# Kernel tuning notes

Hardware: AMD Instinct MI355X
Metric: run time of the kernel (lower is better)

Reference implementation:

```python
import jax, jax.numpy as jnp
import numpy as np

MEM_DIM, H, W = 1024, 16, 16
HW = H * W
N_TOKENS, BATCH = 8192, 8
C1, C2, EPS = 0.01, 0.03, 1e-8


def setup_inputs() -> dict:
    key = jax.random.key(0)
    ks = jax.random.split(key, 5)
    std_w = 1.0 / np.sqrt(HW)
    return {
        "input_tokens": jax.random.normal(ks[0], (N_TOKENS, BATCH, HW), dtype=jnp.float32),
        "memory": jax.random.normal(ks[1], (MEM_DIM, H, W), dtype=jnp.float32) * 0.1,
        "Wq": jax.random.normal(ks[2], (HW, HW), dtype=jnp.float32) * std_w,
        "Wk": jax.random.normal(ks[3], (HW, HW), dtype=jnp.float32) * std_w,
        "Wv": jax.random.normal(ks[4], (HW, HW), dtype=jnp.float32) * std_w,
    }


def _ssim(q, k):
    # q: [N, HW], k: [M, HW] -> ssim: [N, M]
    qm = jnp.mean(q, axis=1, keepdims=True)          # [N,1]
    km = jnp.mean(k, axis=1, keepdims=True)          # [M,1]
    qv = jnp.var(q, axis=1, ddof=1, keepdims=True)   # torch.var unbiased
    kv = jnp.var(k, axis=1, ddof=1, keepdims=True)
    cov = ((q - qm) @ (k - km).T) / (HW - 1)         # [N,M]
    mean_prod = qm @ km.T                            # [N,M]
    numerator = (2.0 * mean_prod + C1) * (2.0 * cov + C2)
    denominator = (qm ** 2 + km.T ** 2 + C1) * (qv + kv.T + C2)
    return numerator / (denominator + EPS)


def reference(input_tokens, memory, Wq, Wk, Wv):
    Nt, B, F = input_tokens.shape
    x = input_tokens.reshape(Nt * B, HW)             # [N, HW]
    q = x @ Wq.T                                     # Linear(bias=False): x @ W^T
    m = memory.reshape(MEM_DIM, HW)
    k = m @ Wk.T
    v = m @ Wv.T
    ssim = _ssim(q, k)                               # [N, MEM_DIM]
    att = jax.nn.softmax(ssim, axis=1)
    out = (att @ v).reshape(Nt, B, F)
    return out
```

## Files before the change

kernel.cpp:

```cpp
#include <hip/hip_runtime.h>
#include <math.h>

typedef __attribute__((ext_vector_type(8)))  short bf16x8;
typedef __attribute__((ext_vector_type(16))) float f32x16;
typedef __attribute__((ext_vector_type(4)))  float f32x4;
typedef __attribute__((ext_vector_type(4)))  unsigned uint4v;

#define MFMA32(a, b, c) __builtin_amdgcn_mfma_f32_32x32x16_bf16((a), (b), (c), 0, 0, 0)

namespace {
constexpr int HWF   = 256;
constexpr int MEMD  = 1024;
constexpr int NROWS = 65536;
constexpr int TM    = 128;
constexpr int NT    = MEMD / 32;
constexpr int THREADS = 256;
constexpr float C1v  = 0.01f;
constexpr float C2v  = 0.03f;
constexpr float EPSv = 1e-8f;
constexpr float RK   = 1.0f / 255.0f;

constexpr int KB0 = 0;
constexpr int KB1 = 16384;
constexpr int VB0 = 32768;
constexpr int VB1 = 49152;
constexpr int STATS = 65536;
constexpr int LRED  = STATS + 12288;
constexpr int SMEM_SZ = LRED + 512;
}

__device__ __forceinline__ short f2bf(float f) {
    union { float f; unsigned u; } v; v.f = f;
    unsigned r = v.u + 0x7fffu + ((v.u >> 16) & 1u);
    return (short)(r >> 16);
}

__device__ __forceinline__ unsigned cvtpk(float a, float b) {
    unsigned r;
    asm("v_cvt_pk_bf16_f32 %0, %1, %2" : "=v"(r) : "v"(a), "v"(b));
    return r;
}

__device__ __forceinline__ void plswap(unsigned &a, unsigned &b) {
#if defined(__has_builtin) && __has_builtin(__builtin_amdgcn_permlane32_swap)
    auto r = __builtin_amdgcn_permlane32_swap((int)a, (int)b, false, false);
    a = (unsigned)r[0]; b = (unsigned)r[1];
#else
    const bool h = (threadIdx.x & 32) != 0;
    const unsigned ax = (unsigned)__shfl_xor((int)a, 32);
    const unsigned bx = (unsigned)__shfl_xor((int)b, 32);
    const unsigned na = h ? bx : a;
    const unsigned nb = h ? b : ax;
    a = na; b = nb;
#endif
}

__device__ __forceinline__ void dma_tile16(const short* gbase, char* smem, int ldsbase,
                                           int wave, int lane) {
    const char* g = (const char*)gbase + wave * 4096 + lane * 16;
    char* l = smem + ldsbase + wave * 4096;
    #pragma unroll
    for (int i = 0; i < 4; ++i) {
        __builtin_amdgcn_global_load_lds(
            (const __attribute__((address_space(1))) unsigned int*)(g + i * 1024),
            (__attribute__((address_space(3))) unsigned int*)(l + i * 1024), 16, 0, 0);
    }
}

__global__ __launch_bounds__(256) void cast_w(
    const float* __restrict__ Wq, const float* __restrict__ Wk,
    const float* __restrict__ Wv, short* __restrict__ wq_bf,
    short* __restrict__ wk_bf, short* __restrict__ wv_bf)
{
    const int b = blockIdx.x, t = threadIdx.x;
    const float* src = (b < 32) ? Wq : (b < 64) ? Wk : Wv;
    short* dst = (b < 32) ? wq_bf : (b < 64) ? wk_bf : wv_bf;
    const int i = (b & 31) * 2048 + t * 8;
    const float4 a = *reinterpret_cast<const float4*>(src + i);
    const float4 c = *reinterpret_cast<const float4*>(src + i + 4);
    uint4v u;
    u[0] = cvtpk(a.x, a.y); u[1] = cvtpk(a.z, a.w);
    u[2] = cvtpk(c.x, c.y); u[3] = cvtpk(c.z, c.w);
    *reinterpret_cast<uint4v*>(dst + i) = u;
}

__global__ __launch_bounds__(256) void prep_mfma(
    const float* __restrict__ mem, const short* __restrict__ wk_bf,
    const short* __restrict__ wv_bf, short* __restrict__ kblob,
    short* __restrict__ vblob, float* __restrict__ sblob)
{
    const int t = threadIdx.x, wave = t >> 6, lane = t & 63;
    const int lo = lane & 31, hi = lane >> 5;
    const bool isV = blockIdx.x >= 8;
    const int jb = (blockIdx.x & 7) * 128 + wave * 32;
    const int j  = jb + lo;

    bf16x8 mB[16];
    {
        const float* mr = mem + (size_t)j * HWF;
        #pragma unroll
        for (int s = 0; s < 16; ++s) {
            const float4 a = *reinterpret_cast<const float4*>(mr + 16 * s + 8 * hi);
            const float4 b = *reinterpret_cast<const float4*>(mr + 16 * s + 8 * hi + 4);
            uint4v u;
            u[0] = cvtpk(a.x, a.y); u[1] = cvtpk(a.z, a.w);
            u[2] = cvtpk(b.x, b.y); u[3] = cvtpk(b.z, b.w);
            mB[s] = __builtin_bit_cast(bf16x8, u);
        }
    }

    const short* W = isV ? wv_bf : wk_bf;
    f32x16 D[8];
    #pragma unroll
    for (int nt = 0; nt < 8; ++nt) D[nt] = (f32x16)(0.f);
    #pragma unroll
    for (int nt = 0; nt < 8; ++nt) {
        #pragma unroll
        for (int s = 0; s < 16; ++s) {
            const bf16x8 wa = *reinterpret_cast<const bf16x8*>(
                W + (size_t)(32 * nt + lo) * HWF + 16 * s + 8 * hi);
            D[nt] = MFMA32(wa, mB[s], D[nt]);
        }
    }

    const int jt = jb >> 5, ro = lo;
    if (!isV) {
        float s = 0.f, ss = 0.f;
        #pragma unroll
        for (int nt = 0; nt < 8; ++nt)
            #pragma unroll
            for (int i = 0; i < 16; ++i) {
                const float v = D[nt][i];
                s += v; ss = __builtin_fmaf(v, v, ss);
            }
        s += __shfl_xor(s, 32);
        ss += __shfl_xor(ss, 32);
        const float km = s * (1.f / HWF);
        const float kv = (ss - s * s * (1.f / HWF)) * (1.f / (HWF - 1));
        #pragma unroll
        for (int nt = 0; nt < 8; ++nt) {
            #pragma unroll
            for (int a = 0; a < 4; ++a) {
                short4 q4;
                q4.x = f2bf(D[nt][4 * a + 0] - km);
                q4.y = f2bf(D[nt][4 * a + 1] - km);
                q4.z = f2bf(D[nt][4 * a + 2] - km);
                q4.w = f2bf(D[nt][4 * a + 3] - km);
                *reinterpret_cast<short4*>(
                    kblob + jt * 8192 + ro * 256 +
                    (((4 * nt + a) ^ (ro & 7)) * 8) + 4 * hi) = q4;
            }
        }
        if (hi == 0) {
            sblob[j]        = 2.f * km;
            sblob[1024 + j] = km * km + C1v;
            sblob[2048 + j] = kv + C2v;
        }
    } else {
        #pragma unroll
        for (int nt = 0; nt < 8; ++nt) {
            #pragma unroll
            for (int i = 0; i < 16; ++i) {
                const int f = 32 * nt + (i & 3) + 8 * (i >> 2) + 4 * hi;
                vblob[jt * 8192 + f * 32 +
                      (((ro >> 3) ^ ((f >> 1) & 3)) * 8) + (ro & 7)] = f2bf(D[nt][i]);
            }
        }
    }
}

__global__ __launch_bounds__(THREADS, 2) void attn(
    const float* __restrict__ x, const short* __restrict__ wq_bf,
    const short* __restrict__ kblob, const short* __restrict__ vblob,
    const float* __restrict__ sblob, float* __restrict__ out)
{
    __shared__ __align__(16) char smem[SMEM_SZ];
    const int t = threadIdx.x, wave = t >> 6, lane = t & 63;
    const int lo = lane & 31, hi = lane >> 5;
    const int rg = wave;
    const int n0 = blockIdx.x * TM;
    const int tok = n0 + 32 * rg + lo;

    dma_tile16(kblob, smem, KB0, wave, lane);
    dma_tile16(vblob, smem, VB0, wave, lane);
    #pragma unroll
    for (int r = 0; r < 3; ++r) {
        __builtin_amdgcn_global_load_lds(
            (const __attribute__((address_space(1))) unsigned int*)
                ((const char*)sblob + r * 4096 + wave * 1024 + lane * 16),
            (__attribute__((address_space(3))) unsigned int*)
                (smem + STATS + r * 4096 + wave * 1024 + lane * 16), 16, 0, 0);
    }

    bf16x8 xB[16];
    {
        const float* xr = x + (size_t)tok * HWF;
        #pragma unroll
        for (int s = 0; s < 16; ++s) {
            const float4 a = *reinterpret_cast<const float4*>(xr + 16 * s + 8 * hi);
            const float4 b = *reinterpret_cast<const float4*>(xr + 16 * s + 8 * hi + 4);
            uint4v u;
            u[0] = cvtpk(a.x, a.y); u[1] = cvtpk(a.z, a.w);
            u[2] = cvtpk(b.x, b.y); u[3] = cvtpk(b.z, b.w);
            xB[s] = __builtin_bit_cast(bf16x8, u);
        }
    }

    f32x16 qD[8];
    #pragma unroll
    for (int nt = 0; nt < 8; ++nt) qD[nt] = (f32x16)(0.f);
    #pragma unroll
    for (int nt = 0; nt < 8; ++nt) {
        #pragma unroll
        for (int s = 0; s < 16; ++s) {
            const bf16x8 wa = *reinterpret_cast<const bf16x8*>(
                wq_bf + (size_t)(32 * nt + lo) * HWF + 16 * s + 8 * hi);
            qD[nt] = MFMA32(wa, xB[s], qD[nt]);
        }
    }

    float qs = 0.f, qss = 0.f;
    #pragma unroll
    for (int nt = 0; nt < 8; ++nt)
        #pragma unroll
        for (int i = 0; i < 16; ++i) {
            const float v = qD[nt][i];
            qs += v; qss = __builtin_fmaf(v, v, qss);
        }
    qs += __shfl_xor(qs, 32);
    qss += __shfl_xor(qss, 32);
    const float qm  = qs * (1.f / HWF);
    const float qv  = (qss - qs * qs * (1.f / HWF)) * (1.f / (HWF - 1));
    const float qm2 = qm * qm;

    bf16x8 qA[16];
    #pragma unroll
    for (int nt = 0; nt < 8; ++nt) {
        unsigned w[8];
        #pragma unroll
        for (int p = 0; p < 8; ++p) w[p] = cvtpk(qD[nt][2 * p], qD[nt][2 * p + 1]);
        #pragma unroll
        for (int h = 0; h < 2; ++h) {
            unsigned a0 = w[4 * h + 0], b0 = w[4 * h + 2];
            unsigned a1 = w[4 * h + 1], b1 = w[4 * h + 3];
            plswap(a0, b0); plswap(a1, b1);
            uint4v u; u[0] = a0; u[1] = a1; u[2] = b0; u[3] = b1;
            qA[2 * nt + h] = __builtin_bit_cast(bf16x8, u);
        }
    }

    f32x16 O4[8];
    #pragma unroll
    for (int ct = 0; ct < 8; ++ct) O4[ct] = (f32x16)(0.f);
    float l = 0.f;
    const int rx = (lo & 7);
    const int vx = (lo >> 1) & 3;

    for (int jt = 0; jt < NT; ++jt) {
        const int cur = jt & 1;
        const int kb = cur ? KB1 : KB0, vb = cur ? VB1 : VB0;
        const int kbn = cur ? KB0 : KB1, vbn = cur ? VB0 : VB1;
        __syncthreads();
        if (jt + 1 < NT) {
            dma_tile16(kblob + (size_t)(jt + 1) * 8192, smem, kbn, wave, lane);
            dma_tile16(vblob + (size_t)(jt + 1) * 8192, smem, vbn, wave, lane);
        }

        f32x16 sacc = (f32x16)(0.f);
        __builtin_amdgcn_s_setprio(1);
        #pragma unroll
        for (int s = 0; s < 16; ++s) {
            const bf16x8 kfr = *reinterpret_cast<const bf16x8*>(
                smem + kb + lo * 512 + (((2 * s + hi) ^ rx) * 16));
            sacc = MFMA32(kfr, qA[s], sacc);
        }
        __builtin_amdgcn_s_setprio(0);

        unsigned pw[8];
        #pragma unroll
        for (int g = 0; g < 4; ++g) {
            const int soff = (32 * jt + 8 * g + 4 * hi) * 4;
            const f32x4 a4 = *reinterpret_cast<const f32x4*>(smem + STATS + soff);
            const f32x4 b4 = *reinterpret_cast<const f32x4*>(smem + STATS + 4096 + soff);
            const f32x4 c4 = *reinterpret_cast<const f32x4*>(smem + STATS + 8192 + soff);
            float pr[4];
            #pragma unroll
            for (int q = 0; q < 4; ++q) {
                const int i = 4 * g + q;
                const float cov2 = __builtin_fmaf(sacc[i], 2.f * RK, C2v);
                const float num  = __builtin_fmaf(a4[q], qm, C1v) * cov2;
                const float den  = __builtin_fmaf(qm2 + b4[q], qv + c4[q], EPSv);
                pr[q] = __expf(__fdividef(num, den));
                l += pr[q];
            }
            pw[2 * g]     = cvtpk(pr[0], pr[1]);
            pw[2 * g + 1] = cvtpk(pr[2], pr[3]);
        }

        #pragma unroll
        for (int h = 0; h < 2; ++h) {
            unsigned a0 = pw[4 * h + 0], b0 = pw[4 * h + 2];
            unsigned a1 = pw[4 * h + 1], b1 = pw[4 * h + 3];
            plswap(a0, b0); plswap(a1, b1);
            uint4v u; u[0] = a0; u[1] = a1; u[2] = b0; u[3] = b1;
            const bf16x8 pa = __builtin_bit_cast(bf16x8, u);
            __builtin_amdgcn_s_setprio(1);
            #pragma unroll
            for (int ct = 0; ct < 8; ++ct) {
                const bf16x8 vfr = *reinterpret_cast<const bf16x8*>(
                    smem + vb + (32 * ct + lo) * 64 + (((2 * h + hi) ^ vx) * 16));
                O4[ct] = MFMA32(pa, vfr, O4[ct]);
            }
            __builtin_amdgcn_s_setprio(0);
        }
    }

    const float lf = l + __shfl_xor(l, 32);
    if (hi == 0)
        *reinterpret_cast<float*>(smem + LRED + (wave * 32 + lo) * 4) = lf;
    float rl[16];
    #pragma unroll
    for (int g = 0; g < 4; ++g) {
        const f32x4 lv = *reinterpret_cast<const f32x4*>(
            smem + LRED + wave * 128 + (8 * g + 4 * hi) * 4);
        rl[4 * g + 0] = 1.f / lv[0];
        rl[4 * g + 1] = 1.f / lv[1];
        rl[4 * g + 2] = 1.f / lv[2];
        rl[4 * g + 3] = 1.f / lv[3];
    }

    #pragma unroll
    for (int ct = 0; ct < 8; ++ct) {
        #pragma unroll
        for (int i = 0; i < 16; ++i) {
            const int row = 32 * rg + (i & 3) + 8 * (i >> 2) + 4 * hi;
            out[(size_t)(n0 + row) * HWF + 32 * ct + lo] = O4[ct][i] * rl[i];
        }
    }
}

extern "C" void kernel_launch(void* const* d_in, const int* in_sizes, int n_in,
                              void* d_out, int out_size, void* d_ws, size_t ws_size,
                              hipStream_t stream) {
    (void)in_sizes; (void)n_in; (void)out_size; (void)ws_size;
    const float* x   = (const float*)d_in[0];
    const float* mem = (const float*)d_in[1];
    const float* Wq  = (const float*)d_in[2];
    const float* Wk  = (const float*)d_in[3];
    const float* Wv  = (const float*)d_in[4];
    float* out = (float*)d_out;

    short* wq_bf = (short*)d_ws;
    short* kblob = wq_bf + 65536;
    short* vblob = kblob + (size_t)MEMD * HWF;
    float* sblob = (float*)(vblob + (size_t)MEMD * HWF);

    short* wk_bf = (short*)out;
    short* wv_bf = wk_bf + 65536;

    cast_w<<<96, 256, 0, stream>>>(Wq, Wk, Wv, wq_bf, wk_bf, wv_bf);
    prep_mfma<<<16, 256, 0, stream>>>(mem, wk_bf, wv_bf, kblob, vblob, sblob);
    attn<<<NROWS / TM, THREADS, 0, stream>>>(x, wq_bf, kblob, vblob, sblob, out);
}
```

Before: 264.8 us.

## Fuse weight cast into K/V projection prep and spread it over more blocks

Merges the separate weight-cast kernel and the K/V projection kernel into one launch. Wk and Wv are now read as fp32 and converted inline, so the intermediate bf16 copies of those weights are gone. The projection work is split across 64 blocks instead of 16, each handling one 32-row memory tile. The per-row mean and variance of K are now reduced across waves through shared memory. This removes one kernel launch and an intermediate round trip, and fills more compute units during prep, at the cost of each block re-reading and re-converting fp32 weights.

Result: faster. 251.2 us (-5.1%).

```diff
diff --git a/kernel.cpp b/kernel.cpp
--- a/kernel.cpp
+++ b/kernel.cpp
@@ -67,33 +67,30 @@
     }
 }
 
-__global__ __launch_bounds__(256) void cast_w(
-    const float* __restrict__ Wq, const float* __restrict__ Wk,
-    const float* __restrict__ Wv, short* __restrict__ wq_bf,
-    short* __restrict__ wk_bf, short* __restrict__ wv_bf)
+__global__ __launch_bounds__(256) void prep(
+    const float* __restrict__ mem, const float* __restrict__ Wq,
+    const float* __restrict__ Wk, const float* __restrict__ Wv,
+    short* __restrict__ wq_bf, short* __restrict__ kblob,
+    short* __restrict__ vblob, float* __restrict__ sblob)
 {
     const int b = blockIdx.x, t = threadIdx.x;
-    const float* src = (b < 32) ? Wq : (b < 64) ? Wk : Wv;
-    short* dst = (b < 32) ? wq_bf : (b < 64) ? wk_bf : wv_bf;
-    const int i = (b & 31) * 2048 + t * 8;
-    const float4 a = *reinterpret_cast<const float4*>(src + i);
-    const float4 c = *reinterpret_cast<const float4*>(src + i + 4);
-    uint4v u;
-    u[0] = cvtpk(a.x, a.y); u[1] = cvtpk(a.z, a.w);
-    u[2] = cvtpk(c.x, c.y); u[3] = cvtpk(c.z, c.w);
-    *reinterpret_cast<uint4v*>(dst + i) = u;
-}
-
-__global__ __launch_bounds__(256) void prep_mfma(
-    const float* __restrict__ mem, const short* __restrict__ wk_bf,
-    const short* __restrict__ wv_bf, short* __restrict__ kblob,
-    short* __restrict__ vblob, float* __restrict__ sblob)
-{
-    const int t = threadIdx.x, wave = t >> 6, lane = t & 63;
+    if (b >= 64) {
+        const int i = (b - 64) * 2048 + t * 8;
+        const float4 a = *reinterpret_cast<const float4*>(Wq + i);
+        const float4 c = *reinterpret_cast<const float4*>(Wq + i + 4);
+        uint4v u;
+        u[0] = cvtpk(a.x, a.y); u[1] = cvtpk(a.z, a.w);
+        u[2] = cvtpk(c.x, c.y); u[3] = cvtpk(c.z, c.w);
+        *reinterpret_cast<uint4v*>(wq_bf + i) = u;
+        return;
+    }
+
+    __shared__ float2 redS[4][32];
+    const bool isV = b >= 32;
+    const int jt = b & 31;
+    const int w = t >> 6, lane = t & 63;
     const int lo = lane & 31, hi = lane >> 5;
-    const bool isV = blockIdx.x >= 8;
-    const int jb = (blockIdx.x & 7) * 128 + wave * 32;
-    const int j  = jb + lo;
+    const int j = 32 * jt + lo;
 
     bf16x8 mB[16];
     {
@@ -101,69 +98,84 @@
         #pragma unroll
         for (int s = 0; s < 16; ++s) {
             const float4 a = *reinterpret_cast<const float4*>(mr + 16 * s + 8 * hi);
-            const float4 b = *reinterpret_cast<const float4*>(mr + 16 * s + 8 * hi + 4);
+            const float4 c = *reinterpret_cast<const float4*>(mr + 16 * s + 8 * hi + 4);
             uint4v u;
             u[0] = cvtpk(a.x, a.y); u[1] = cvtpk(a.z, a.w);
-            u[2] = cvtpk(b.x, b.y); u[3] = cvtpk(b.z, b.w);
+            u[2] = cvtpk(c.x, c.y); u[3] = cvtpk(c.z, c.w);
             mB[s] = __builtin_bit_cast(bf16x8, u);
         }
     }
 
-    const short* W = isV ? wv_bf : wk_bf;
-    f32x16 D[8];
-    #pragma unroll
-    for (int nt = 0; nt < 8; ++nt) D[nt] = (f32x16)(0.f);
-    #pragma unroll
-    for (int nt = 0; nt < 8; ++nt) {
-        #pragma unroll
-        for (int s = 0; s < 16; ++s) {
-            const bf16x8 wa = *reinterpret_cast<const bf16x8*>(
-                W + (size_t)(32 * nt + lo) * HWF + 16 * s + 8 * hi);
-            D[nt] = MFMA32(wa, mB[s], D[nt]);
-        }
-    }
-
-    const int jt = jb >> 5, ro = lo;
+    const float* Wsrc = isV ? Wv : Wk;
+    f32x16 D[2];
+    D[0] = (f32x16)(0.f); D[1] = (f32x16)(0.f);
+    #pragma unroll
+    for (int n2 = 0; n2 < 2; ++n2) {
+        const int nt = 2 * w + n2;
+        const float* wr = Wsrc + (size_t)(32 * nt + lo) * HWF;
+        #pragma unroll
+        for (int s = 0; s < 16; ++s) {
+            const float4 a = *reinterpret_cast<const float4*>(wr + 16 * s + 8 * hi);
+            const float4 c = *reinterpret_cast<const float4*>(wr + 16 * s + 8 * hi + 4);
+            uint4v u;
+            u[0] = cvtpk(a.x, a.y); u[1] = cvtpk(a.z, a.w);
+            u[2] = cvtpk(c.x, c.y); u[3] = cvtpk(c.z, c.w);
+            const bf16x8 wa = __builtin_bit_cast(bf16x8, u);
+            D[n2] = MFMA32(wa, mB[s], D[n2]);
+        }
+    }
+
     if (!isV) {
         float s = 0.f, ss = 0.f;
         #pragma unroll
-        for (int nt = 0; nt < 8; ++nt)
+        for (int n2 = 0; n2 < 2; ++n2)
             #pragma unroll
             for (int i = 0; i < 16; ++i) {
-                const float v = D[nt][i];
+                const float v = D[n2][i];
                 s += v; ss = __builtin_fmaf(v, v, ss);
             }
         s += __shfl_xor(s, 32);
         ss += __shfl_xor(ss, 32);
-        const float km = s * (1.f / HWF);
-        const float kv = (ss - s * s * (1.f / HWF)) * (1.f / (HWF - 1));
-        #pragma unroll
-        for (int nt = 0; nt < 8; ++nt) {
+        if (hi == 0) redS[w][lo] = make_float2(s, ss);
+        __syncthreads();
+        float st = 0.f, sst = 0.f;
+        #pragma unroll
+        for (int ww = 0; ww < 4; ++ww) {
+            const float2 p = redS[ww][lo];
+            st += p.x; sst += p.y;
+        }
+        const float km = st * (1.f / HWF);
+        const float kv = (sst - st * st * (1.f / HWF)) * (1.f / (HWF - 1));
+
+        #pragma unroll
+        for (int n2 = 0; n2 < 2; ++n2) {
+            const int nt = 2 * w + n2;
             #pragma unroll
             for (int a = 0; a < 4; ++a) {
                 short4 q4;
-                q4.x = f2bf(D[nt][4 * a + 0] - km);
-                q4.y = f2bf(D[nt][4 * a + 1] - km);
-                q4.z = f2bf(D[nt][4 * a + 2] - km);
-                q4.w = f2bf(D[nt][4 * a + 3] - km);
+                q4.x = f2bf(D[n2][4 * a + 0] - km);
+                q4.y = f2bf(D[n2][4 * a + 1] - km);
+                q4.z = f2bf(D[n2][4 * a + 2] - km);
+                q4.w = f2bf(D[n2][4 * a + 3] - km);
                 *reinterpret_cast<short4*>(
-                    kblob + jt * 8192 + ro * 256 +
-                    (((4 * nt + a) ^ (ro & 7)) * 8) + 4 * hi) = q4;
-            }
-        }
-        if (hi == 0) {
+                    kblob + jt * 8192 + lo * 256 +
+                    (((4 * nt + a) ^ (lo & 7)) * 8) + 4 * hi) = q4;
+            }
+        }
+        if (w == 0 && hi == 0) {
             sblob[j]        = 2.f * km;
             sblob[1024 + j] = km * km + C1v;
             sblob[2048 + j] = kv + C2v;
         }
     } else {
         #pragma unroll
-        for (int nt = 0; nt < 8; ++nt) {
+        for (int n2 = 0; n2 < 2; ++n2) {
+            const int nt = 2 * w + n2;
             #pragma unroll
             for (int i = 0; i < 16; ++i) {
                 const int f = 32 * nt + (i & 3) + 8 * (i >> 2) + 4 * hi;
                 vblob[jt * 8192 + f * 32 +
-                      (((ro >> 3) ^ ((f >> 1) & 3)) * 8) + (ro & 7)] = f2bf(D[nt][i]);
+                      (((lo >> 3) ^ ((f >> 1) & 3)) * 8) + (lo & 7)] = f2bf(D[n2][i]);
             }
         }
     }
@@ -355,10 +367,6 @@
     short* vblob = kblob + (size_t)MEMD * HWF;
     float* sblob = (float*)(vblob + (size_t)MEMD * HWF);
 
-    short* wk_bf = (short*)out;
-    short* wv_bf = wk_bf + 65536;
-
-    cast_w<<<96, 256, 0, stream>>>(Wq, Wk, Wv, wq_bf, wk_bf, wv_bf);
-    prep_mfma<<<16, 256, 0, stream>>>(mem, wk_bf, wv_bf, kblob, vblob, sblob);
+    prep<<<96, 256, 0, stream>>>(mem, Wq, Wk, Wv, wq_bf, kblob, vblob, sblob);
     attn<<<NROWS / TM, THREADS, 0, stream>>>(x, wq_bf, kblob, vblob, sblob, out);
 }
```
